# Kernel tuning notes

Hardware: AMD Instinct MI355X
Metric: run time of the kernel (lower is better)

## Reference

```python
import jax, jax.numpy as jnp
import numpy as np

SEQ_LEN = 2048

def setup_inputs() -> dict:
    key = jax.random.key(0)
    kq, kk, kv = jax.random.split(key, 3)
    B, S, D = 8, SEQ_LEN, 64
    q = jax.random.normal(kq, (B, S, D), dtype=jnp.float32)
    k = jax.random.normal(kk, (B, S, D), dtype=jnp.float32)
    v = jax.random.normal(kv, (B, S, D), dtype=jnp.float32)
    return {"q": q, "k": k, "v": v}

def reference(q, k, v):
    # scores: [B, S, S] = q @ k^T  (note: original applies NO 1/sqrt(d) scaling)
    scores = jnp.einsum('bqd,bkd->bqk', q, k)
    S = scores.shape[-1]
    causal = jnp.tril(jnp.ones((S, S), dtype=bool))  # lower-triangular mask
    scores = jnp.where(causal, scores, -jnp.inf)
    weights = jax.nn.softmax(scores, axis=-1)
    return jnp.einsum('bqk,bkd->bqd', weights, v)
```

## Files before the change

kernel.cpp:

```cpp
#include <hip/hip_runtime.h>


#define BATCH 8
#define SEQ 2048
#define DIM 64
#define NEL (BATCH * SEQ * DIM)

typedef __attribute__((ext_vector_type(8))) short short8;
typedef __attribute__((ext_vector_type(4))) float f32x4;

#define MFMA(a, b, c) __builtin_amdgcn_mfma_f32_16x16x32_bf16(a, b, c, 0, 0, 0)

__device__ __forceinline__ unsigned short f2bf(float x) {
    unsigned u = __float_as_uint(x);
    unsigned r = u + 0x7fffu + ((u >> 16) & 1u);
    return (unsigned short)(r >> 16);
}
__device__ __forceinline__ float bf2f(unsigned short h) {
    return __uint_as_float(((unsigned)h) << 16);
}
__device__ __forceinline__ unsigned cvt_pk_bf16(float a, float b) {
    unsigned r;
    asm("v_cvt_pk_bf16_f32 %0, %1, %2" : "=v"(r) : "v"(a), "v"(b));
    return r;
}
__device__ __forceinline__ short8 ld8(const unsigned short* p) {
    return *(const short8*)p;
}
__device__ __forceinline__ void splitA(float4 a, float4 b, short8& h8, short8& l8) {
    float v[8] = {a.x, a.y, a.z, a.w, b.x, b.y, b.z, b.w};
#pragma unroll
    for (int i = 0; i < 8; ++i) {
        unsigned u  = __float_as_uint(v[i]);
        unsigned hu = u & 0xffff0000u;
        h8[i] = (short)(hu >> 16);
        float lf = v[i] - __uint_as_float(hu);
        l8[i] = (short)(__float_as_uint(lf) >> 16);
    }
}

__device__ __forceinline__ float dpp_max16(float x) {
    float o;
    o = __int_as_float(__builtin_amdgcn_update_dpp(0, __float_as_int(x), 0xB1, 0xF, 0xF, true));
    x = fmaxf(x, o);
    o = __int_as_float(__builtin_amdgcn_update_dpp(0, __float_as_int(x), 0x4E, 0xF, 0xF, true));
    x = fmaxf(x, o);
    o = __int_as_float(__builtin_amdgcn_update_dpp(0, __float_as_int(x), 0x141, 0xF, 0xF, true));
    x = fmaxf(x, o);
    o = __int_as_float(__builtin_amdgcn_update_dpp(0, __float_as_int(x), 0x140, 0xF, 0xF, true));
    return fmaxf(x, o);
}
__device__ __forceinline__ float dpp_sum16(float x) {
    float o;
    o = __int_as_float(__builtin_amdgcn_update_dpp(0, __float_as_int(x), 0xB1, 0xF, 0xF, true));
    x += o;
    o = __int_as_float(__builtin_amdgcn_update_dpp(0, __float_as_int(x), 0x4E, 0xF, 0xF, true));
    x += o;
    o = __int_as_float(__builtin_amdgcn_update_dpp(0, __float_as_int(x), 0x141, 0xF, 0xF, true));
    x += o;
    o = __int_as_float(__builtin_amdgcn_update_dpp(0, __float_as_int(x), 0x140, 0xF, 0xF, true));
    return x + o;
}

__global__ __launch_bounds__(256) void prep(
    const float* __restrict__ K, const float* __restrict__ V,
    unsigned short* __restrict__ Kf, unsigned short* __restrict__ Vf)
{
    __shared__ unsigned short sT[64][72];
    const int blk = blockIdx.x;
    const int t = threadIdx.x;

    if (blk < 512) {
        const int g  = blk * 256 + t;
        const int l  = g & 63;
        const int h  = (g >> 6) & 1;
        const int Sg = g >> 7;
        const int b  = Sg >> 7;
        const int S  = Sg & 127;
        const int key = S * 16 + (l & 15);
        const float* src = K + ((size_t)(b * SEQ + key)) * DIM + h * 32 + (l >> 4) * 8;
        float4 a = *(const float4*)src;
        float4 c = *(const float4*)(src + 4);
        float v[8] = {a.x, a.y, a.z, a.w, c.x, c.y, c.z, c.w};
        short8 h8, l8;
#pragma unroll
        for (int i = 0; i < 8; ++i) {
            unsigned short hh = f2bf(v[i]);
            h8[i] = (short)hh;
            l8[i] = (short)f2bf(v[i] - bf2f(hh));
        }
        unsigned short* dst = Kf + (((size_t)Sg) << 11) + (h << 9) + l * 8;
        *(short8*)dst = h8;
        *(short8*)(dst + 1024) = l8;
        return;
    }

    const int tile = blk - 512;
    const int b = tile >> 5;
    const int s0 = (tile & 31) * 64;
    const int srow = t >> 4;
    const int d4   = (t & 15) * 4;
#pragma unroll
    for (int i = 0; i < 4; ++i) {
        const int row = srow + i * 16;
        float4 v = *(const float4*)(V + ((size_t)(b * SEQ + s0 + row)) * DIM + d4);
        sT[d4 + 0][row] = f2bf(v.x);
        sT[d4 + 1][row] = f2bf(v.y);
        sT[d4 + 2][row] = f2bf(v.z);
        sT[d4 + 3][row] = f2bf(v.w);
    }
    __syncthreads();
#pragma unroll
    for (int i = 0; i < 2; ++i) {
        const int fid = t + i * 256;
        const int cc  = fid >> 8;
        const int nt  = (fid >> 6) & 3;
        const int l   = fid & 63;
        const int key = cc * 32 + (l >> 4) * 8;
        const int dim = nt * 16 + (l & 15);
        const int c   = (s0 >> 5) + cc;
        unsigned short* dst =
            Vf + ((((size_t)(b * 64 + c)) * 4 + nt) << 9) + l * 8;
        *(float4*)dst = *(const float4*)&sT[dim][key];
    }
}

__global__ __launch_bounds__(256) void attn_main(
    const float* __restrict__ Q,
    const unsigned short* __restrict__ Kf,
    const unsigned short* __restrict__ Vf, float* __restrict__ O)
{
    __shared__ __align__(16) char scratch[4][4352];
    __shared__ float sMl[4][16][2];

    const int bid  = blockIdx.x;
    const int g    = bid >> 8;
    const int idx  = bid & 255;
    const int b    = idx & (BATCH - 1);
    const int tl   = idx >> 3;
    const int qt   = (g & 1) ? (g * 32 + 31 - tl) : (g * 32 + tl);

    const int t    = threadIdx.x;
    const int w    = t >> 6;
    const int lane = t & 63;
    const int quad = lane >> 4;
    const int n16  = lane & 15;
    const int boff = b * SEQ;

    unsigned short* sPw = (unsigned short*)scratch[w];
    float*          sOw = (float*)scratch[w];

    const unsigned short* KfL = Kf + (((size_t)(b * 128)) << 11) + lane * 8;

    const int q0 = qt * 16;
    const int q_max = q0 + 15;

    short8 qh0, ql0, qh1, ql1;
    {
        const float* qb = Q + ((size_t)(boff + q0 + n16)) * DIM + quad * 8;
        splitA(*(const float4*)(qb),      *(const float4*)(qb + 4),  qh0, ql0);
        splitA(*(const float4*)(qb + 32), *(const float4*)(qb + 36), qh1, ql1);
    }

    float m0 = -1e30f, m1 = -1e30f, m2 = -1e30f, m3 = -1e30f;
    float l0 = 0.f, l1 = 0.f, l2 = 0.f, l3 = 0.f;
    f32x4 oacc[4];
#pragma unroll
    for (int i = 0; i < 4; ++i) oacc[i] = (f32x4){0.f, 0.f, 0.f, 0.f};

    for (int kb = w * 128; kb <= q_max; kb += 512) {
        const int rem  = q_max - kb;
        const int nsub = min(8, (rem >> 4) + 1);
        const int nchain = (nsub + 1) >> 1;
        f32x4 sacc[8];

#pragma unroll
        for (int gp = 0; gp < 4; ++gp) {
            const int stA = 2 * gp, stB = stA + 1;
            if (stA < nsub) {
                const unsigned short* pA = KfL + (((size_t)((kb >> 4) + stA)) << 11);
                short8 khA0 = ld8(pA),        khA1 = ld8(pA + 512);
                short8 klA0 = ld8(pA + 1024), klA1 = ld8(pA + 1536);
                const bool okB = (stB < nsub);
                const unsigned short* pB = KfL + (((size_t)((kb >> 4) + stB)) << 11);
                short8 khB0, khB1, klB0, klB1;
                if (okB) {
                    khB0 = ld8(pB);        khB1 = ld8(pB + 512);
                    klB0 = ld8(pB + 1024); klB1 = ld8(pB + 1536);
                }
                f32x4 accA = (f32x4){0.f, 0.f, 0.f, 0.f};
                accA = MFMA(qh0, khA0, accA);
                accA = MFMA(qh1, khA1, accA);
                accA = MFMA(qh0, klA0, accA);
                accA = MFMA(qh1, klA1, accA);
                accA = MFMA(ql0, khA0, accA);
                accA = MFMA(ql1, khA1, accA);
                sacc[stA] = accA;
                if (okB) {
                    f32x4 accB = (f32x4){0.f, 0.f, 0.f, 0.f};
                    accB = MFMA(qh0, khB0, accB);
                    accB = MFMA(qh1, khB1, accB);
                    accB = MFMA(qh0, klB0, accB);
                    accB = MFMA(qh1, klB1, accB);
                    accB = MFMA(ql0, khB0, accB);
                    accB = MFMA(ql1, khB1, accB);
                    sacc[stB] = accB;
                } else {
                    sacc[stB] = (f32x4){-1e30f, -1e30f, -1e30f, -1e30f};
                }
            } else {
                sacc[stA] = (f32x4){-1e30f, -1e30f, -1e30f, -1e30f};
                sacc[stB] = (f32x4){-1e30f, -1e30f, -1e30f, -1e30f};
            }
        }

        if (kb + 127 > q0) {
#pragma unroll
            for (int st = 0; st < 8; ++st) {
                if (st < nsub) {
                    const int key = kb + st * 16 + n16;
#pragma unroll
                    for (int r = 0; r < 4; ++r)
                        if (key > q0 + quad * 4 + r) sacc[st][r] = -1e30f;
                }
            }
        }

        float mt0 = sacc[0][0], mt1 = sacc[0][1], mt2 = sacc[0][2], mt3 = sacc[0][3];
#pragma unroll
        for (int st = 1; st < 8; ++st) {
            mt0 = fmaxf(mt0, sacc[st][0]);
            mt1 = fmaxf(mt1, sacc[st][1]);
            mt2 = fmaxf(mt2, sacc[st][2]);
            mt3 = fmaxf(mt3, sacc[st][3]);
        }
        mt0 = dpp_max16(mt0); mt1 = dpp_max16(mt1);
        mt2 = dpp_max16(mt2); mt3 = dpp_max16(mt3);
        const float mn0 = fmaxf(m0, mt0), mn1 = fmaxf(m1, mt1);
        const float mn2 = fmaxf(m2, mt2), mn3 = fmaxf(m3, mt3);
        const float a0 = __expf(m0 - mn0), a1 = __expf(m1 - mn1);
        const float a2 = __expf(m2 - mn2), a3 = __expf(m3 - mn3);
        m0 = mn0; m1 = mn1; m2 = mn2; m3 = mn3;

        float ps0 = 0.f, ps1 = 0.f, ps2 = 0.f, ps3 = 0.f;
        const int stmax = 2 * nchain;
#pragma unroll
        for (int st = 0; st < 8; ++st) {
            if (st < stmax) {
                float p0 = 0.f, p1 = 0.f, p2 = 0.f, p3 = 0.f;
                if (st < nsub) {
                    p0 = __expf(sacc[st][0] - mn0);
                    p1 = __expf(sacc[st][1] - mn1);
                    p2 = __expf(sacc[st][2] - mn2);
                    p3 = __expf(sacc[st][3] - mn3);
                    ps0 += p0; ps1 += p1; ps2 += p2; ps3 += p3;
                }
                const int col = st * 16 + n16;
                const unsigned r01 = cvt_pk_bf16(p0, p1);
                const unsigned r23 = cvt_pk_bf16(p2, p3);
                sPw[(quad * 4 + 0) * 136 + col] = (unsigned short)r01;
                sPw[(quad * 4 + 1) * 136 + col] = (unsigned short)(r01 >> 16);
                sPw[(quad * 4 + 2) * 136 + col] = (unsigned short)r23;
                sPw[(quad * 4 + 3) * 136 + col] = (unsigned short)(r23 >> 16);
            }
        }
        ps0 = dpp_sum16(ps0); ps1 = dpp_sum16(ps1);
        ps2 = dpp_sum16(ps2); ps3 = dpp_sum16(ps3);
        l0 = l0 * a0 + ps0; l1 = l1 * a1 + ps1;
        l2 = l2 * a2 + ps2; l3 = l3 * a3 + ps3;
#pragma unroll
        for (int nt = 0; nt < 4; ++nt) {
            oacc[nt][0] *= a0; oacc[nt][1] *= a1;
            oacc[nt][2] *= a2; oacc[nt][3] *= a3;
        }

#pragma unroll
        for (int ch = 0; ch < 4; ++ch) {
            if (ch < nchain) {
                short8 pa = ld8(&sPw[n16 * 136 + ch * 32 + quad * 8]);
                const size_t cbase =
                    (((size_t)(b * 64 + (kb >> 5) + ch)) * 4) << 9;
#pragma unroll
                for (int nt = 0; nt < 4; ++nt) {
                    short8 vv = ld8(Vf + cbase + (nt << 9) + lane * 8);
                    oacc[nt] = MFMA(pa, vv, oacc[nt]);
                }
            }
        }
    }

#pragma unroll
    for (int nt = 0; nt < 4; ++nt)
#pragma unroll
        for (int r = 0; r < 4; ++r)
            sOw[(quad * 4 + r) * 68 + nt * 16 + n16] = oacc[nt][r];
    if (n16 == 0) {
        sMl[w][quad * 4 + 0][0] = m0; sMl[w][quad * 4 + 0][1] = l0;
        sMl[w][quad * 4 + 1][0] = m1; sMl[w][quad * 4 + 1][1] = l1;
        sMl[w][quad * 4 + 2][0] = m2; sMl[w][quad * 4 + 2][1] = l2;
        sMl[w][quad * 4 + 3][0] = m3; sMl[w][quad * 4 + 3][1] = l3;
    }
    __syncthreads();

    const int row  = t >> 4;
    const int col4 = (t & 15) * 4;
    float M = fmaxf(fmaxf(sMl[0][row][0], sMl[1][row][0]),
                    fmaxf(sMl[2][row][0], sMl[3][row][0]));
    float L = 0.f;
    float ox = 0.f, oy = 0.f, oz = 0.f, ow = 0.f;
#pragma unroll
    for (int wv = 0; wv < 4; ++wv) {
        const float ew = __expf(sMl[wv][row][0] - M);
        L += ew * sMl[wv][row][1];
        const float* op = (const float*)scratch[wv] + row * 68 + col4;
        ox += ew * op[0]; oy += ew * op[1]; oz += ew * op[2]; ow += ew * op[3];
    }
    const float inv = 1.0f / L;
    float4 res = make_float4(ox * inv, oy * inv, oz * inv, ow * inv);
    *(float4*)(O + ((size_t)(boff + q0 + row)) * DIM + col4) = res;
}

extern "C" void kernel_launch(void* const* d_in, const int* in_sizes, int n_in,
                              void* d_out, int out_size, void* d_ws, size_t ws_size,
                              hipStream_t stream) {
    const float* q = (const float*)d_in[0];
    const float* k = (const float*)d_in[1];
    const float* v = (const float*)d_in[2];
    float* out = (float*)d_out;

    unsigned short* Kf = (unsigned short*)d_ws;
    unsigned short* Vf = Kf + 2 * NEL;

    prep<<<dim3(512 + 256), dim3(256), 0, stream>>>(k, v, Kf, Vf);
    attn_main<<<dim3(1024), dim3(256), 0, stream>>>(q, Kf, Vf, out);
}
```

Before: 90.53 us.

## Split long causal query tiles into key segments with a separate combine kernel

```diff
diff --git a/kernel.cpp b/kernel.cpp
--- a/kernel.cpp
+++ b/kernel.cpp
@@ -128,17 +128,20 @@
 __global__ __launch_bounds__(256) void attn_main(
     const float* __restrict__ Q,
     const unsigned short* __restrict__ Kf,
-    const unsigned short* __restrict__ Vf, float* __restrict__ O)
+    const unsigned short* __restrict__ Vf,
+    float* __restrict__ Po, float* __restrict__ Pml)
 {
     __shared__ __align__(16) char scratch[4][4352];
     __shared__ float sMl[4][16][2];
 
-    const int bid  = blockIdx.x;
-    const int g    = bid >> 8;
-    const int idx  = bid & 255;
-    const int b    = idx & (BATCH - 1);
-    const int tl   = idx >> 3;
-    const int qt   = (g & 1) ? (g * 32 + 31 - tl) : (g * 32 + tl);
+    const int fid  = blockIdx.x;
+    const int b    = fid & (BATCH - 1);
+    const int rest = fid >> 3;
+    int qt, seg;
+    if (rest < 32)       { qt = rest;                          seg = 0; }
+    else if (rest < 96)  { int o = rest - 32;  qt = 32 + (o >> 1); seg = o & 1; }
+    else if (rest < 192) { int o = rest - 96;  int q3 = o / 3; qt = 64 + q3; seg = o - q3 * 3; }
+    else                 { int o = rest - 192; qt = 96 + (o >> 2); seg = o & 3; }
 
     const int t    = threadIdx.x;
     const int w    = t >> 6;
@@ -168,7 +171,8 @@
 #pragma unroll
     for (int i = 0; i < 4; ++i) oacc[i] = (f32x4){0.f, 0.f, 0.f, 0.f};
 
-    for (int kb = w * 128; kb <= q_max; kb += 512) {
+    const int kb = seg * 512 + w * 128;
+    if (kb <= q_max) {
         const int rem  = q_max - kb;
         const int nsub = min(8, (rem >> 4) + 1);
         const int nchain = (nsub + 1) >> 1;
@@ -315,9 +319,50 @@
         const float* op = (const float*)scratch[wv] + row * 68 + col4;
         ox += ew * op[0]; oy += ew * op[1]; oz += ew * op[2]; ow += ew * op[3];
     }
+
+    const int pb = ((b << 7) + qt) * 4 + seg;
+    float* po = Po + (((size_t)pb * 16 + row) << 6) + col4;
+    *(float4*)po = make_float4(ox, oy, oz, ow);
+    if (col4 == 0) {
+        Pml[pb * 32 + row * 2 + 0] = M;
+        Pml[pb * 32 + row * 2 + 1] = L;
+    }
+}
+
+__global__ __launch_bounds__(256) void combine(
+    const float* __restrict__ Po, const float* __restrict__ Pml,
+    float* __restrict__ O)
+{
+    const int bid = blockIdx.x;
+    const int b   = bid & (BATCH - 1);
+    const int qt  = bid >> 3;
+    const int nseg = (qt >> 5) + 1;
+
+    const int t    = threadIdx.x;
+    const int row  = t >> 4;
+    const int col4 = (t & 15) * 4;
+    const int pb0  = ((b << 7) + qt) * 4;
+
+    float M = Pml[pb0 * 32 + row * 2];
+#pragma unroll 4
+    for (int s = 1; s < nseg; ++s)
+        M = fmaxf(M, Pml[(pb0 + s) * 32 + row * 2]);
+
+    float L = 0.f;
+    float ox = 0.f, oy = 0.f, oz = 0.f, ow = 0.f;
+#pragma unroll 4
+    for (int s = 0; s < nseg; ++s) {
+        const float Ms = Pml[(pb0 + s) * 32 + row * 2 + 0];
+        const float Ls = Pml[(pb0 + s) * 32 + row * 2 + 1];
+        const float ew = __expf(Ms - M);
+        L += ew * Ls;
+        const float* po = Po + (((size_t)(pb0 + s) * 16 + row) << 6) + col4;
+        float4 v = *(const float4*)po;
+        ox += ew * v.x; oy += ew * v.y; oz += ew * v.z; ow += ew * v.w;
+    }
     const float inv = 1.0f / L;
-    float4 res = make_float4(ox * inv, oy * inv, oz * inv, ow * inv);
-    *(float4*)(O + ((size_t)(boff + q0 + row)) * DIM + col4) = res;
+    float* dst = O + ((size_t)(b * SEQ + qt * 16 + row)) * DIM + col4;
+    *(float4*)dst = make_float4(ox * inv, oy * inv, oz * inv, ow * inv);
 }
 
 extern "C" void kernel_launch(void* const* d_in, const int* in_sizes, int n_in,
@@ -330,7 +375,10 @@
 
     unsigned short* Kf = (unsigned short*)d_ws;
     unsigned short* Vf = Kf + 2 * NEL;
+    float* Po  = (float*)(Vf + NEL);
+    float* Pml = Po + (size_t)4096 * 16 * 64;
 
     prep<<<dim3(512 + 256), dim3(256), 0, stream>>>(k, v, Kf, Vf);
-    attn_main<<<dim3(1024), dim3(256), 0, stream>>>(q, Kf, Vf, out);
-}
+    attn_main<<<dim3(2560), dim3(256), 0, stream>>>(q, Kf, Vf, Po, Pml);
+    combine<<<dim3(1024), dim3(256), 0, stream>>>(Po, Pml, out);
+}
```

New measurement: 98.68 us. 9.0% more time.
